# Kernel optimization log

Hardware: AMD Instinct MI355X
Metric: run time of the kernel (lower is better)

Reference implementation:

```python
import jax, jax.numpy as jnp
import numpy as np

B, NPG, HID, HEADS, L = 8, 512, 128, 8, 4
N = B * NPG
E = 16384
EDIM = HID // 4  # edge_dim = hidden_dim // 4 = 32


def _ln(x, g, b):
    m = x.mean(-1, keepdims=True)
    v = ((x - m) ** 2).mean(-1, keepdims=True)
    return (x - m) / jnp.sqrt(v + 1e-5) * g + b


def setup_inputs() -> dict:
    key = jax.random.key(0)
    ks = jax.random.split(key, 24)
    s = 0.05
    epg = E // B
    base = jnp.repeat(jnp.arange(B) * NPG, epg)
    src = base + jax.random.randint(ks[0], (E,), 0, NPG)
    dst = base + jax.random.randint(ks[1], (E,), 0, NPG)
    d = {
        'x': jax.random.randint(ks[2], (N, 1), 0, 100),
        'edge_index': jnp.stack([src, dst]),
        'edge_attr': jax.random.normal(ks[3], (E, 1), jnp.float32),
        'batch': jnp.repeat(jnp.arange(B), NPG),
        'atom_emb': jax.random.normal(ks[4], (100, HID)) * s,
        'edge_w': jax.random.normal(ks[5], (1, EDIM)) * s,
        'edge_b': jnp.zeros((EDIM,)),
        'wq': jax.random.normal(ks[6], (L, HID, HEADS * HID)) * s,
        'bq': jnp.zeros((L, HEADS * HID)),
        'wk': jax.random.normal(ks[7], (L, HID, HEADS * HID)) * s,
        'bk': jnp.zeros((L, HEADS * HID)),
        'wv': jax.random.normal(ks[8], (L, HID, HEADS * HID)) * s,
        'bv': jnp.zeros((L, HEADS * HID)),
        'we': jax.random.normal(ks[9], (L, EDIM, HEADS * HID)) * s,
        'wskip': jax.random.normal(ks[10], (L, HID, HID)) * s,
        'bskip': jnp.zeros((L, HID)),
        'ln_g': jnp.ones((L, HID)),
        'ln_b': jnp.zeros((L, HID)),
        'mha_in_w': jax.random.normal(ks[11], (HID, 3 * HID)) * s,
        'mha_in_b': jnp.zeros((3 * HID,)),
        'mha_out_w': jax.random.normal(ks[12], (HID, HID)) * s,
        'mha_out_b': jnp.zeros((HID,)),
        'w1': jax.random.normal(ks[13], (HID, HID)) * s,
        'b1': jnp.zeros((HID,)),
        'w2': jax.random.normal(ks[14], (HID, HID // 2)) * s,
        'b2': jnp.zeros((HID // 2,)),
        'w3': jax.random.normal(ks[15], (HID // 2, 3)) * s,
        'b3': jnp.zeros((3,)),
    }
    return d


def reference(x, edge_index, edge_attr, batch, atom_emb, edge_w, edge_b,
              wq, bq, wk, bk, wv, bv, we, wskip, bskip, ln_g, ln_b,
              mha_in_w, mha_in_b, mha_out_w, mha_out_b, w1, b1, w2, b2, w3, b3):
    src, dst = edge_index[0], edge_index[1]
    h = atom_emb[x[:, 0]]                       # [N, HID]
    e = edge_attr @ edge_w + edge_b             # [E, EDIM]
    scale = 1.0 / jnp.sqrt(jnp.float32(HID))    # per-head channel dim = HID
    for i in range(L):
        res = h
        q = (h @ wq[i] + bq[i]).reshape(N, HEADS, HID)
        k = (h @ wk[i] + bk[i]).reshape(N, HEADS, HID)
        v = (h @ wv[i] + bv[i]).reshape(N, HEADS, HID)
        ee = (e @ we[i]).reshape(E, HEADS, HID)
        kj = k[src] + ee                        # [E, HEADS, HID]
        vj = v[src] + ee
        logits = jnp.einsum('ehd,ehd->eh', q[dst], kj) * scale
        m = jax.ops.segment_max(logits, dst, num_segments=N)
        a = jnp.exp(logits - m[dst])
        z = jax.ops.segment_sum(a, dst, num_segments=N)
        a = a / (z[dst] + 1e-16)                # edge softmax per target node
        agg = jax.ops.segment_sum(a[:, :, None] * vj, dst, num_segments=N)
        out = agg.mean(axis=1) + h @ wskip[i] + bskip[i]  # concat=False + root skip
        h = jax.nn.gelu(_ln(out + res, ln_g[i], ln_b[i]), approximate=False)
    # equal-size graphs: ragged->padded conversion is a plain reshape, no padding
    p = h.reshape(B, NPG, HID)
    qkv = p @ mha_in_w + mha_in_b               # [B, n, 3*HID]
    hd = HID // HEADS
    q, k, v = [t.reshape(B, NPG, HEADS, hd).transpose(0, 2, 1, 3)
               for t in jnp.split(qkv, 3, axis=-1)]
    att = jax.nn.softmax(jnp.einsum('bhqd,bhkd->bhqk', q, k) / jnp.sqrt(jnp.float32(hd)), axis=-1)
    o = jnp.einsum('bhqk,bhkd->bhqd', att, v).transpose(0, 2, 1, 3).reshape(B, NPG, HID)
    o = (o @ mha_out_w + mha_out_b).reshape(N, HID)
    y = jax.nn.gelu(o @ w1 + b1, approximate=False)
    y = jax.nn.gelu(y @ w2 + b2, approximate=False)
    return y @ w3 + b3                          # [N, 3]
```

## Files before the change

kernel.cpp:

```cpp
#include <hip/hip_runtime.h>
#include <hip/hip_bf16.h>
#include <math.h>

#define NN 4096
#define NE 16384
#define NLAYERS 4

#define WT_STRIDE 442368

typedef __attribute__((ext_vector_type(8))) short bf16x8;
typedef __attribute__((ext_vector_type(4))) float floatx4;

__device__ __forceinline__ float gelu_f(float x) {
  return 0.5f * x * (1.0f + erff(x * 0.70710678118654752440f));
}

__device__ __forceinline__ void bsplit(float a, unsigned short& hi, unsigned short& lo) {
  __hip_bfloat16 h16 = __float2bfloat16(a);
  hi = *(unsigned short*)&h16;
  const float r = a - __bfloat162float(h16);
  __hip_bfloat16 l16 = __float2bfloat16(r);
  lo = *(unsigned short*)&l16;
}

union F16U { float4 v4[4]; float f[16]; };

__global__ void k_init(const int* __restrict__ x, const float* __restrict__ atom_emb,
                       const float* __restrict__ edge_attr, const float* __restrict__ edge_w,
                       const float* __restrict__ edge_b, float* __restrict__ h,
                       float* __restrict__ ef, int* __restrict__ counts,
                       unsigned short* __restrict__ hhi, unsigned short* __restrict__ hlo) {
  const int idx = blockIdx.x * 256 + threadIdx.x;
  const float hv = atom_emb[x[idx >> 7] * 128 + (idx & 127)];
  h[idx] = hv;
  bsplit(hv, hhi[idx], hlo[idx]);
  ef[idx] = edge_attr[idx >> 5] * edge_w[idx & 31] + edge_b[idx & 31];
  if (idx < NN) counts[idx] = 0;
}

__global__ void k_hist(const int* __restrict__ eidx, int* __restrict__ counts) {
  const int e = blockIdx.x * 256 + threadIdx.x;
  if (e < NE) atomicAdd(&counts[eidx[NE + e]], 1);
}

__global__ void k_scan(const int* __restrict__ counts, int* __restrict__ offs,
                       int* __restrict__ heads) {
  __shared__ int tmp[1024];
  const int t = threadIdx.x;
  const int c0 = counts[t*4], c1 = counts[t*4+1], c2 = counts[t*4+2], c3 = counts[t*4+3];
  const int s = c0 + c1 + c2 + c3;
  tmp[t] = s; __syncthreads();
  for (int off = 1; off < 1024; off <<= 1) {
    int v = (t >= off) ? tmp[t - off] : 0;
    __syncthreads();
    tmp[t] += v;
    __syncthreads();
  }
  int base = tmp[t] - s;
  offs[t*4]   = base;                heads[t*4]   = base;
  offs[t*4+1] = base + c0;           heads[t*4+1] = base + c0;
  offs[t*4+2] = base + c0 + c1;      heads[t*4+2] = base + c0 + c1;
  offs[t*4+3] = base + c0 + c1 + c2; heads[t*4+3] = base + c0 + c1 + c2;
  if (t == 1023) offs[NN] = tmp[1023];
}

__global__ void k_scatter(const int* __restrict__ eidx, int* __restrict__ heads,
                          int* __restrict__ elist) {
  const int e = blockIdx.x * 256 + threadIdx.x;
  if (e < NE) {
    int p = atomicAdd(&heads[eidx[NE + e]], 1);
    elist[p] = e;
  }
}

__global__ __launch_bounds__(256) void k_wcvt(
    const float* __restrict__ wq, const float* __restrict__ wk,
    const float* __restrict__ wv, const float* __restrict__ wsk,
    unsigned short* __restrict__ wthi, unsigned short* __restrict__ wtlo) {
  const int z = blockIdx.z;
  const int layer = z >> 2, mat = z & 3;
  int NC; const float* W; int woff;
  if (mat == 0)      { NC = 1024; W = wq  + (size_t)layer * 131072; woff = 0; }
  else if (mat == 1) { NC = 1024; W = wk  + (size_t)layer * 131072; woff = 131072; }
  else if (mat == 2) { NC = 1024; W = wv  + (size_t)layer * 131072; woff = 262144; }
  else               { NC = 128;  W = wsk + (size_t)layer * 16384;  woff = 393216; }
  const int c0 = blockIdx.x * 64;
  if (c0 >= NC) return;
  const int k0 = blockIdx.y * 64;
  __shared__ unsigned short th[64][65], tl[64][65];
  const int t = threadIdx.x;
  for (int i = t; i < 4096; i += 256) {
    const int kk = i >> 6, c = i & 63;
    bsplit(W[(size_t)(k0 + kk) * NC + c0 + c], th[kk][c], tl[kk][c]);
  }
  __syncthreads();
  unsigned short* oh = wthi + (size_t)layer * WT_STRIDE + woff;
  unsigned short* ol = wtlo + (size_t)layer * WT_STRIDE + woff;
  for (int i = t; i < 4096; i += 256) {
    const int n = i >> 6, k = i & 63;
    oh[(size_t)(c0 + n) * 128 + k0 + k] = th[k][n];
    ol[(size_t)(c0 + n) * 128 + k0 + k] = tl[k][n];
  }
}

__global__ __launch_bounds__(256) void k_wqe(
    const float* __restrict__ wq, const float* __restrict__ bq,
    const float* __restrict__ we, unsigned short* __restrict__ wthi,
    unsigned short* __restrict__ wtlo, float* __restrict__ bqe) {
  const int layer = blockIdx.x >> 3, hh = blockIdx.x & 7;
  const float* wq_l = wq + (size_t)layer * 131072;
  const float* we_l = we + (size_t)layer * 32768;
  const float* bq_l = bq + (size_t)layer * 1024;
  __shared__ float wqS[128][132];
  __shared__ float weS[32][132];
  const int t = threadIdx.x;
  for (int i = t; i < 4096; i += 256) {
    const int d = i >> 5, dd4 = (i & 31) << 2;
    *(float4*)&wqS[d][dd4] = *(const float4*)&wq_l[(size_t)d * 1024 + hh * 128 + dd4];
  }
  for (int i = t; i < 1024; i += 256) {
    const int c = i >> 5, dd4 = (i & 31) << 2;
    *(float4*)&weS[c][dd4] = *(const float4*)&we_l[(size_t)c * 1024 + hh * 128 + dd4];
  }
  __syncthreads();
  const int d = t & 127, cg = t >> 7;
  float acc[16];
  #pragma unroll
  for (int cc = 0; cc < 16; cc++) acc[cc] = 0.f;
  for (int dd = 0; dd < 128; dd++) {
    const float a = wqS[d][dd];
    #pragma unroll
    for (int cc = 0; cc < 16; cc++)
      acc[cc] += a * weS[cg * 16 + cc][dd];
  }
  unsigned short* oh = wthi + (size_t)layer * WT_STRIDE + 409600;
  unsigned short* ol = wtlo + (size_t)layer * WT_STRIDE + 409600;
  #pragma unroll
  for (int cc = 0; cc < 16; cc++) {
    const int j = hh * 32 + cg * 16 + cc;
    unsigned short hi, lo;
    bsplit(acc[cc], hi, lo);
    oh[(size_t)j * 128 + d] = hi;
    ol[(size_t)j * 128 + d] = lo;
  }
  if (t < 32) {
    float s = 0.f;
    for (int dd = 0; dd < 128; dd++) s += bq_l[hh * 128 + dd] * weS[t][dd];
    bqe[layer * 256 + hh * 32 + t] = s;
  }
}

__global__ __launch_bounds__(256) void k_mfqkv(
    const unsigned short* __restrict__ hhi, const unsigned short* __restrict__ hlo,
    const unsigned short* __restrict__ wth, const unsigned short* __restrict__ wtl,
    const float* __restrict__ bq, const float* __restrict__ bk,
    const float* __restrict__ bv, const float* __restrict__ bsk,
    const float* __restrict__ bqe_l,
    float* __restrict__ qb, float* __restrict__ kb,
    float* __restrict__ vb, float* __restrict__ skb, float* __restrict__ qeb) {
  const int z = blockIdx.z;
  int NC; const float* bias; float* C; int woff;
  if (z == 0)      { NC = 1024; bias = bq;    C = qb;  woff = 0; }
  else if (z == 1) { NC = 1024; bias = bk;    C = kb;  woff = 131072; }
  else if (z == 2) { NC = 1024; bias = bv;    C = vb;  woff = 262144; }
  else if (z == 3) { NC = 128;  bias = bsk;   C = skb; woff = 393216; }
  else             { NC = 256;  bias = bqe_l; C = qeb; woff = 409600; }
  const int c0 = blockIdx.x * 64;
  if (c0 >= NC) return;
  __shared__ unsigned short Ah[64][136], Al[64][136], Wh[64][136], Wl[64][136];
  const int t = threadIdx.x;
  const int n0 = blockIdx.y * 64;
  for (int i = t; i < 1024; i += 256) {
    const int r = i >> 4, c8 = (i & 15) << 3;
    *(uint4*)&Ah[r][c8] = *(const uint4*)&hhi[(size_t)(n0 + r) * 128 + c8];
    *(uint4*)&Al[r][c8] = *(const uint4*)&hlo[(size_t)(n0 + r) * 128 + c8];
    *(uint4*)&Wh[r][c8] = *(const uint4*)&wth[woff + (size_t)(c0 + r) * 128 + c8];
    *(uint4*)&Wl[r][c8] = *(const uint4*)&wtl[woff + (size_t)(c0 + r) * 128 + c8];
  }
  __syncthreads();
  const int w = t >> 6, l = t & 63;
  const int quad = l >> 4, lm = l & 15;
  floatx4 acc[4] = {{0.f,0.f,0.f,0.f},{0.f,0.f,0.f,0.f},{0.f,0.f,0.f,0.f},{0.f,0.f,0.f,0.f}};
  #pragma unroll
  for (int kc = 0; kc < 4; kc++) {
    const int ko = kc * 32 + quad * 8;
    const bf16x8 ah = *(const bf16x8*)&Ah[w * 16 + lm][ko];
    const bf16x8 al = *(const bf16x8*)&Al[w * 16 + lm][ko];
    #pragma unroll
    for (int ct = 0; ct < 4; ct++) {
      const bf16x8 bh = *(const bf16x8*)&Wh[ct * 16 + lm][ko];
      const bf16x8 bl = *(const bf16x8*)&Wl[ct * 16 + lm][ko];
      acc[ct] = __builtin_amdgcn_mfma_f32_16x16x32_bf16(ah, bh, acc[ct], 0, 0, 0);
      acc[ct] = __builtin_amdgcn_mfma_f32_16x16x32_bf16(ah, bl, acc[ct], 0, 0, 0);
      acc[ct] = __builtin_amdgcn_mfma_f32_16x16x32_bf16(al, bh, acc[ct], 0, 0, 0);
    }
  }
  #pragma unroll
  for (int ct = 0; ct < 4; ct++) {
    const int col = c0 + ct * 16 + lm;
    const float bb = bias[col];
    #pragma unroll
    for (int r = 0; r < 4; r++) {
      const int row = n0 + w * 16 + quad * 4 + r;
      C[(size_t)row * NC + col] = acc[ct][r] + bb;
    }
  }
}

__global__ __launch_bounds__(256) void k_gemm2(const float* __restrict__ A,
                                               const float* __restrict__ W,
                                               const float* __restrict__ bias,
                                               float* __restrict__ C, int NC, int gelu) {
  __shared__ float As[128][65];
  __shared__ float Ws[128][64];
  const int t = threadIdx.x;
  const int n0 = blockIdx.y * 64, c0 = blockIdx.x * 64;
  for (int i = t; i < 2048; i += 256) {
    const int r = i & 63, k4 = (i >> 6) << 2;
    const float4 a = *(const float4*)&A[(size_t)(n0 + r) * 128 + k4];
    As[k4+0][r] = a.x; As[k4+1][r] = a.y; As[k4+2][r] = a.z; As[k4+3][r] = a.w;
  }
  for (int i = t; i < 2048; i += 256) {
    const int kk = i >> 4, c4 = (i & 15) << 2;
    *(float4*)&Ws[kk][c4] = *(const float4*)&W[(size_t)kk * NC + c0 + c4];
  }
  __syncthreads();
  const int tr = (t >> 4) << 2;
  const int tc = (t & 15) << 2;
  float acc[4][4];
  #pragma unroll
  for (int i = 0; i < 4; i++)
    #pragma unroll
    for (int j = 0; j < 4; j++) acc[i][j] = 0.f;
  #pragma unroll 8
  for (int k = 0; k < 128; k++) {
    const float4 av = *(const float4*)&As[k][tr];
    const float4 wv = *(const float4*)&Ws[k][tc];
    acc[0][0] += av.x*wv.x; acc[0][1] += av.x*wv.y; acc[0][2] += av.x*wv.z; acc[0][3] += av.x*wv.w;
    acc[1][0] += av.y*wv.x; acc[1][1] += av.y*wv.y; acc[1][2] += av.y*wv.z; acc[1][3] += av.y*wv.w;
    acc[2][0] += av.z*wv.x; acc[2][1] += av.z*wv.y; acc[2][2] += av.z*wv.z; acc[2][3] += av.z*wv.w;
    acc[3][0] += av.w*wv.x; acc[3][1] += av.w*wv.y; acc[3][2] += av.w*wv.z; acc[3][3] += av.w*wv.w;
  }
  const float4 bb = *(const float4*)&bias[c0 + tc];
  #pragma unroll
  for (int i = 0; i < 4; i++) {
    float4 v;
    v.x = acc[i][0] + bb.x; v.y = acc[i][1] + bb.y;
    v.z = acc[i][2] + bb.z; v.w = acc[i][3] + bb.w;
    if (gelu) { v.x = gelu_f(v.x); v.y = gelu_f(v.y); v.z = gelu_f(v.z); v.w = gelu_f(v.w); }
    *(float4*)&C[(size_t)(n0 + tr + i) * NC + c0 + tc] = v;
  }
}

__global__ __launch_bounds__(256) void k_corr(const float* __restrict__ sbuf,
                                              const float* __restrict__ we_l,
                                              float* __restrict__ corrb) {
  __shared__ float As[32][256];
  __shared__ float Ws[128][64];
  const int t = threadIdx.x;
  const int n0 = blockIdx.y * 32, c0 = blockIdx.x * 64;
  for (int i = t; i < 2048; i += 256) {
    const int r = i >> 6, c4 = (i & 63) << 2;
    *(float4*)&As[r][c4] = *(const float4*)&sbuf[(size_t)(n0 + r) * 256 + c4];
  }
  const int tx = t & 63, ty = t >> 6;
  float acc[8] = {0.f,0.f,0.f,0.f,0.f,0.f,0.f,0.f};
  for (int kc = 0; kc < 2; kc++) {
    __syncthreads();
    for (int i = t; i < 2048; i += 256) {
      const int kk = i >> 4, c4 = (i & 15) << 2;
      const int k = kc * 128 + kk;
      const int hh = k >> 5, c = k & 31;
      *(float4*)&Ws[kk][c4] = *(const float4*)&we_l[(size_t)c * 1024 + hh * 128 + c0 + c4];
    }
    __syncthreads();
    for (int kk = 0; kk < 128; kk += 4) {
      const float w0 = Ws[kk+0][tx];
      const float w1 = Ws[kk+1][tx];
      const float w2 = Ws[kk+2][tx];
      const float w3 = Ws[kk+3][tx];
      #pragma unroll
      for (int j = 0; j < 8; j++) {
        const float4 a = *(const float4*)&As[ty*8 + j][kc*128 + kk];
        acc[j] += a.x*w0 + a.y*w1 + a.z*w2 + a.w*w3;
      }
    }
  }
  #pragma unroll
  for (int j = 0; j < 8; j++)
    corrb[(size_t)(n0 + ty*8 + j) * 128 + c0 + tx] = acc[j];
}

__global__ __launch_bounds__(64) void k_edge(const float* __restrict__ qb,
                                             const float* __restrict__ kb,
                                             const float* __restrict__ vb,
                                             const float* __restrict__ qe,
                                             const float* __restrict__ ef,
                                             const int* __restrict__ offs,
                                             const int* __restrict__ elist,
                                             const int* __restrict__ eidx,
                                             float* __restrict__ accm,
                                             float* __restrict__ sbuf) {
  const int n = blockIdx.x;
  const int lane = threadIdx.x;
  const int hh = lane >> 3, s8 = lane & 7;
  const int d0 = hh * 128 + s8 * 16;
  F16U qv;
  {
    const float4* qp = (const float4*)(qb + (size_t)n * 1024 + d0);
    #pragma unroll
    for (int i = 0; i < 4; i++) qv.v4[i] = qp[i];
  }
  const float4 qe4 = *(const float4*)(qe + (size_t)n * 256 + hh * 32 + s8 * 4);
  float m = -INFINITY, z = 0.f;
  float acc[16];
  #pragma unroll
  for (int i = 0; i < 16; i++) acc[i] = 0.f;
  float sx = 0.f, sy = 0.f, sz = 0.f, sw = 0.f;
  const int e0 = offs[n], e1 = offs[n + 1];
  for (int tt = e0; tt < e1; tt++) {
    const int e = elist[tt];
    const int src = eidx[e];
    F16U kv;
    {
      const float4* kp = (const float4*)(kb + (size_t)src * 1024 + d0);
      #pragma unroll
      for (int i = 0; i < 4; i++) kv.v4[i] = kp[i];
    }
    const float4 ef4 = *(const float4*)(ef + (size_t)e * 32 + s8 * 4);
    float p0 = qe4.x*ef4.x + qe4.y*ef4.y;
    float p1 = qe4.z*ef4.z + qe4.w*ef4.w;
    float p2 = 0.f, p3 = 0.f;
    #pragma unroll
    for (int i = 0; i < 4; i++) {
      p0 += qv.f[i]      * kv.f[i];
      p1 += qv.f[4 + i]  * kv.f[4 + i];
      p2 += qv.f[8 + i]  * kv.f[8 + i];
      p3 += qv.f[12 + i] * kv.f[12 + i];
    }
    float p = (p0 + p1) + (p2 + p3);
    p += __shfl_xor(p, 1);
    p += __shfl_xor(p, 2);
    p += __shfl_xor(p, 4);
    const float logit = p * 0.08838834764831845f;
    if (logit > m + 8.f) {
      const float f = __expf(m - logit);
      z *= f; sx *= f; sy *= f; sz *= f; sw *= f;
      #pragma unroll
      for (int i = 0; i < 16; i++) acc[i] *= f;
      m = logit;
    }
    const float w = __expf(logit - m);
    z += w;
    F16U vv;
    {
      const float4* vp = (const float4*)(vb + (size_t)src * 1024 + d0);
      #pragma unroll
      for (int i = 0; i < 4; i++) vv.v4[i] = vp[i];
    }
    #pragma unroll
    for (int i = 0; i < 16; i++) acc[i] += w * vv.f[i];
    sx += w * ef4.x; sy += w * ef4.y;
    sz += w * ef4.z; sw += w * ef4.w;
  }
  const float inv = 1.f / (z + 1e-16f);
  *(float4*)(sbuf + (size_t)n * 256 + hh * 32 + s8 * 4) =
      make_float4(sx * inv, sy * inv, sz * inv, sw * inv);
  F16U ov;
  #pragma unroll
  for (int i = 0; i < 16; i++) ov.f[i] = acc[i] * inv;
  #pragma unroll
  for (int mask = 8; mask <= 32; mask <<= 1)
    #pragma unroll
    for (int i = 0; i < 16; i++) ov.f[i] += __shfl_xor(ov.f[i], mask);
  if (hh == 0) {
    #pragma unroll
    for (int i = 0; i < 16; i++) ov.f[i] *= 0.125f;
    float4* ap = (float4*)(accm + (size_t)n * 128 + s8 * 16);
    #pragma unroll
    for (int i = 0; i < 4; i++) ap[i] = ov.v4[i];
  }
}

__global__ __launch_bounds__(128) void k_post2(float* __restrict__ h,
                                               const float* __restrict__ accm,
                                               const float* __restrict__ corrb,
                                               const float* __restrict__ skb,
                                               const float* __restrict__ lng,
                                               const float* __restrict__ lnb,
                                               unsigned short* __restrict__ hhi,
                                               unsigned short* __restrict__ hlo) {
  const int n = blockIdx.x, d = threadIdx.x;
  __shared__ float red[128], stat[2];
  const size_t o = (size_t)n * 128 + d;
  const float out = accm[o] + 0.125f * corrb[o] + skb[o] + h[o];
  red[d] = out; __syncthreads();
  for (int s2 = 64; s2 > 0; s2 >>= 1) { if (d < s2) red[d] += red[d + s2]; __syncthreads(); }
  if (d == 0) stat[0] = red[0] * (1.f / 128.f);
  __syncthreads();
  const float mean = stat[0];
  const float dev = out - mean;
  red[d] = dev * dev; __syncthreads();
  for (int s2 = 64; s2 > 0; s2 >>= 1) { if (d < s2) red[d] += red[d + s2]; __syncthreads(); }
  if (d == 0) stat[1] = red[0] * (1.f / 128.f);
  __syncthreads();
  const float var = stat[1];
  const float y = dev / sqrtf(var + 1e-5f) * lng[d] + lnb[d];
  const float g = gelu_f(y);
  h[o] = g;
  bsplit(g, hhi[o], hlo[o]);
}

__global__ __launch_bounds__(256) void k_attn2b(const float* __restrict__ qkvm,
                                                float* __restrict__ pm,
                                                float* __restrict__ pz,
                                                float* __restrict__ pacc) {
  __shared__ float ks2[64][16];
  __shared__ float vs2[64][16];
  const int ksp = blockIdx.x, qt = blockIdx.y, bh = blockIdx.z;
  const int b = bh >> 3, hh = bh & 7;
  const int t = threadIdx.x;
  const size_t rbase = (size_t)(b * 512 + ksp * 64);
  {
    const int j = t >> 2, d4 = (t & 3) << 2;
    const size_t ro = (rbase + j) * 384 + hh * 16 + d4;
    *(float4*)&ks2[j][d4] = *(const float4*)&qkvm[ro + 128];
    *(float4*)&vs2[j][d4] = *(const float4*)&qkvm[ro + 256];
  }
  __syncthreads();
  const int qrow = qt * 256 + t;
  const int nq = b * 512 + qrow;
  F16U qv;
  {
    const float4* qp = (const float4*)(qkvm + (size_t)nq * 384 + hh * 16);
    #pragma unroll
    for (int i = 0; i < 4; i++) qv.v4[i] = qp[i];
  }
  float m = -INFINITY, z = 0.f;
  float acc[16];
  #pragma unroll
  for (int i = 0; i < 16; i++) acc[i] = 0.f;
  for (int j = 0; j < 64; j += 2) {
    F16U k0, k1, v0, v1;
    {
      const float4* p0 = (const float4*)ks2[j];
      const float4* p1 = (const float4*)ks2[j + 1];
      const float4* q0 = (const float4*)vs2[j];
      const float4* q1 = (const float4*)vs2[j + 1];
      #pragma unroll
      for (int i = 0; i < 4; i++) {
        k0.v4[i] = p0[i]; k1.v4[i] = p1[i];
        v0.v4[i] = q0[i]; v1.v4[i] = q1[i];
      }
    }
    float a0 = 0.f, a1 = 0.f, a2 = 0.f, a3 = 0.f;
    float b0 = 0.f, b1 = 0.f, b2 = 0.f, b3 = 0.f;
    #pragma unroll
    for (int i = 0; i < 4; i++) {
      a0 += qv.f[i]      * k0.f[i];
      a1 += qv.f[4 + i]  * k0.f[4 + i];
      a2 += qv.f[8 + i]  * k0.f[8 + i];
      a3 += qv.f[12 + i] * k0.f[12 + i];
      b0 += qv.f[i]      * k1.f[i];
      b1 += qv.f[4 + i]  * k1.f[4 + i];
      b2 += qv.f[8 + i]  * k1.f[8 + i];
      b3 += qv.f[12 + i] * k1.f[12 + i];
    }
    const float sa = ((a0 + a1) + (a2 + a3)) * 0.25f;
    const float sb = ((b0 + b1) + (b2 + b3)) * 0.25f;
    const float smax = fmaxf(sa, sb);
    if (smax > m + 8.f) {
      const float f = __expf(m - smax);
      z *= f;
      #pragma unroll
      for (int i = 0; i < 16; i++) acc[i] *= f;
      m = smax;
    }
    const float wa = __expf(sa - m);
    const float wb = __expf(sb - m);
    z += wa + wb;
    #pragma unroll
    for (int i = 0; i < 16; i++)
      acc[i] += wa * v0.f[i] + wb * v1.f[i];
  }
  const int p = (bh * 512 + qrow) * 8 + ksp;
  pm[p] = m; pz[p] = z;
  float4* pp = (float4*)&pacc[(size_t)p * 16];
  F16U ov;
  #pragma unroll
  for (int i = 0; i < 16; i++) ov.f[i] = acc[i];
  #pragma unroll
  for (int i = 0; i < 4; i++) pp[i] = ov.v4[i];
}

__global__ void k_amerge(const float* __restrict__ pm, const float* __restrict__ pz,
                         const float* __restrict__ pacc, float* __restrict__ ob) {
  const int idx = blockIdx.x * 256 + threadIdx.x;
  if (idx >= 32768) return;
  const int bh = idx >> 9, qrow = idx & 511;
  const int b = bh >> 3, hh = bh & 7;
  float ms = pm[idx*8];
  #pragma unroll
  for (int s = 1; s < 8; s++) ms = fmaxf(ms, pm[idx*8+s]);
  float wgt[8];
  float z = 0.f;
  #pragma unroll
  for (int s = 0; s < 8; s++) {
    wgt[s] = __expf(pm[idx*8+s] - ms);
    z += pz[idx*8+s] * wgt[s];
  }
  const float inv = 1.f / z;
  float* op = &ob[(size_t)(b * 512 + qrow) * 128 + hh * 16];
  #pragma unroll
  for (int d = 0; d < 16; d++) {
    float o = 0.f;
    #pragma unroll
    for (int s = 0; s < 8; s++)
      o += pacc[(size_t)(idx*8+s) * 16 + d] * wgt[s];
    op[d] = o * inv;
  }
}

__global__ void k_final(const float* __restrict__ y2, const float* __restrict__ w3,
                        const float* __restrict__ b3, float* __restrict__ out) {
  const int idx = blockIdx.x * 256 + threadIdx.x;
  if (idx >= NN * 3) return;
  const int n = idx / 3, j = idx % 3;
  float s = b3[j];
  const float* yp = y2 + (size_t)n * 64;
  #pragma unroll
  for (int c = 0; c < 64; c++) s += yp[c] * w3[c * 3 + j];
  out[idx] = s;
}

extern "C" void kernel_launch(void* const* d_in, const int* in_sizes, int n_in,
                              void* d_out, int out_size, void* d_ws, size_t ws_size,
                              hipStream_t stream) {
  const int*   x         = (const int*)d_in[0];
  const int*   eidx      = (const int*)d_in[1];
  const float* edge_attr = (const float*)d_in[2];
  const float* atom_emb  = (const float*)d_in[4];
  const float* edge_w    = (const float*)d_in[5];
  const float* edge_b    = (const float*)d_in[6];
  const float* wq        = (const float*)d_in[7];
  const float* bq        = (const float*)d_in[8];
  const float* wk        = (const float*)d_in[9];
  const float* bk        = (const float*)d_in[10];
  const float* wv        = (const float*)d_in[11];
  const float* bv        = (const float*)d_in[12];
  const float* we        = (const float*)d_in[13];
  const float* wskip     = (const float*)d_in[14];
  const float* bskip     = (const float*)d_in[15];
  const float* ln_g      = (const float*)d_in[16];
  const float* ln_b      = (const float*)d_in[17];
  const float* mha_in_w  = (const float*)d_in[18];
  const float* mha_in_b  = (const float*)d_in[19];
  const float* mha_out_w = (const float*)d_in[20];
  const float* mha_out_b = (const float*)d_in[21];
  const float* w1        = (const float*)d_in[22];
  const float* b1        = (const float*)d_in[23];
  const float* w2        = (const float*)d_in[24];
  const float* b2        = (const float*)d_in[25];
  const float* w3        = (const float*)d_in[26];
  const float* b3        = (const float*)d_in[27];

  float* ws   = (float*)d_ws;
  float* h    = ws;
  float* ef   = h + 524288;
  float* qb   = ef + 524288;
  float* kb   = qb + 4194304;
  float* vb   = kb + 4194304;
  float* qe   = vb + 4194304;
  float* big  = qe + 1048576;
  float* accm = big;
  float* corrb= big + 524288;
  float* skb  = big + 1048576;
  unsigned short* hhi  = (unsigned short*)(big + 1572864);
  unsigned short* hlo  = hhi + 524288;
  unsigned short* wthi = hlo + 524288;
  unsigned short* wtlo = wthi + 1769472;
  float* sbuf = big + 4194304;
  float* qkvm = qb;
  float* pm   = sbuf;
  float* pz   = sbuf + 262144;
  float* pacc = big;
  float* ob   = kb;
  float* mo   = kb + 524288;
  float* y1   = kb + 1048576;
  float* y2   = kb + 1572864;
  int* counts = (int*)(sbuf + 1048576);
  int* offs   = counts + 4100;
  int* heads  = offs + 4100;
  int* elist  = heads + 4100;
  float* bqe  = (float*)(elist + 16384);

  k_init<<<2048, 256, 0, stream>>>(x, atom_emb, edge_attr, edge_w, edge_b, h, ef, counts,
                                   hhi, hlo);
  k_hist<<<64, 256, 0, stream>>>(eidx, counts);
  k_scan<<<1, 1024, 0, stream>>>(counts, offs, heads);
  k_scatter<<<64, 256, 0, stream>>>(eidx, heads, elist);
  k_wcvt<<<dim3(16, 2, 16), 256, 0, stream>>>(wq, wk, wv, wskip, wthi, wtlo);
  k_wqe<<<32, 256, 0, stream>>>(wq, bq, we, wthi, wtlo, bqe);

  for (int i = 0; i < NLAYERS; i++) {
    const float* bq_i  = bq + (size_t)i * 1024;
    const float* bk_i  = bk + (size_t)i * 1024;
    const float* bv_i  = bv + (size_t)i * 1024;
    const float* we_i  = we + (size_t)i * 32768;
    const float* bsk_i = bskip + (size_t)i * 128;
    const float* g_i   = ln_g + (size_t)i * 128;
    const float* b_i   = ln_b + (size_t)i * 128;
    const unsigned short* wth_i = wthi + (size_t)i * WT_STRIDE;
    const unsigned short* wtl_i = wtlo + (size_t)i * WT_STRIDE;

    k_mfqkv<<<dim3(16, 64, 5), 256, 0, stream>>>(hhi, hlo, wth_i, wtl_i,
                                                 bq_i, bk_i, bv_i, bsk_i, bqe + i * 256,
                                                 qb, kb, vb, skb, qe);
    k_edge<<<4096, 64, 0, stream>>>(qb, kb, vb, qe, ef, offs, elist, eidx, accm, sbuf);
    k_corr<<<dim3(2, 128), 256, 0, stream>>>(sbuf, we_i, corrb);
    k_post2<<<4096, 128, 0, stream>>>(h, accm, corrb, skb, g_i, b_i, hhi, hlo);
  }

  k_gemm2<<<dim3(6, 64), 256, 0, stream>>>(h, mha_in_w, mha_in_b, qkvm, 384, 0);
  k_attn2b<<<dim3(8, 2, 64), 256, 0, stream>>>(qkvm, pm, pz, pacc);
  k_amerge<<<128, 256, 0, stream>>>(pm, pz, pacc, ob);
  k_gemm2<<<dim3(2, 64), 256, 0, stream>>>(ob, mha_out_w, mha_out_b, mo, 128, 0);
  k_gemm2<<<dim3(2, 64), 256, 0, stream>>>(mo, w1, b1, y1, 128, 1);
  k_gemm2<<<dim3(1, 64), 256, 0, stream>>>(y1, w2, b2, y2, 64, 1);
  k_final<<<48, 256, 0, stream>>>(y2, w3, b3, (float*)d_out);
}
```

Measured before the change: 553.3 us.

## Fuse edge-correction GEMM with LayerNorm/GELU post, compact QKV grid, batch edge warps

Merges the per-layer correction GEMM and the residual+LayerNorm+GELU post-processing into one kernel, so the corrb buffer is no longer written and re-read and one launch per layer goes away. The QKV projection grid is flattened to cover only the 54 valid column tiles instead of launching 80 with early exits. The edge kernel now packs four nodes per 256-thread block with a strided node mapping. The fused post kernel runs on only 128 blocks and redoes the correction GEMM for both column halves inside each block, so there is less parallelism for that stage.

Measured after the change: 561.0 us. Within noise of the previous version (+1.4%).

```diff
diff --git a/kernel.cpp b/kernel.cpp
--- a/kernel.cpp
+++ b/kernel.cpp
@@ -158,15 +158,13 @@
     const float* __restrict__ bqe_l,
     float* __restrict__ qb, float* __restrict__ kb,
     float* __restrict__ vb, float* __restrict__ skb, float* __restrict__ qeb) {
-  const int z = blockIdx.z;
-  int NC; const float* bias; float* C; int woff;
-  if (z == 0)      { NC = 1024; bias = bq;    C = qb;  woff = 0; }
-  else if (z == 1) { NC = 1024; bias = bk;    C = kb;  woff = 131072; }
-  else if (z == 2) { NC = 1024; bias = bv;    C = vb;  woff = 262144; }
-  else if (z == 3) { NC = 128;  bias = bsk;   C = skb; woff = 393216; }
-  else             { NC = 256;  bias = bqe_l; C = qeb; woff = 409600; }
-  const int c0 = blockIdx.x * 64;
-  if (c0 >= NC) return;
+  const int xb = blockIdx.x;
+  int NC; const float* bias; float* C; int woff; int c0;
+  if (xb < 16)      { NC = 1024; bias = bq;    C = qb;  woff = 0;      c0 = xb * 64; }
+  else if (xb < 32) { NC = 1024; bias = bk;    C = kb;  woff = 131072; c0 = (xb-16) * 64; }
+  else if (xb < 48) { NC = 1024; bias = bv;    C = vb;  woff = 262144; c0 = (xb-32) * 64; }
+  else if (xb < 50) { NC = 128;  bias = bsk;   C = skb; woff = 393216; c0 = (xb-48) * 64; }
+  else              { NC = 256;  bias = bqe_l; C = qeb; woff = 409600; c0 = (xb-50) * 64; }
   __shared__ unsigned short Ah[64][136], Al[64][136], Wh[64][136], Wl[64][136];
   const int t = threadIdx.x;
   const int n0 = blockIdx.y * 64;
@@ -252,57 +250,99 @@
   }
 }
 
-__global__ __launch_bounds__(256) void k_corr(const float* __restrict__ sbuf,
-                                              const float* __restrict__ we_l,
-                                              float* __restrict__ corrb) {
+__global__ __launch_bounds__(256) void k_corrpost(
+    const float* __restrict__ sbuf, const float* __restrict__ we_l,
+    const float* __restrict__ accm, const float* __restrict__ skb,
+    const float* __restrict__ lng, const float* __restrict__ lnb,
+    float* __restrict__ h,
+    unsigned short* __restrict__ hhi, unsigned short* __restrict__ hlo) {
   __shared__ float As[32][256];
   __shared__ float Ws[128][64];
+  __shared__ float sC[32][129];
   const int t = threadIdx.x;
-  const int n0 = blockIdx.y * 32, c0 = blockIdx.x * 64;
+  const int n0 = blockIdx.x * 32;
   for (int i = t; i < 2048; i += 256) {
     const int r = i >> 6, c4 = (i & 63) << 2;
     *(float4*)&As[r][c4] = *(const float4*)&sbuf[(size_t)(n0 + r) * 256 + c4];
   }
   const int tx = t & 63, ty = t >> 6;
-  float acc[8] = {0.f,0.f,0.f,0.f,0.f,0.f,0.f,0.f};
-  for (int kc = 0; kc < 2; kc++) {
-    __syncthreads();
-    for (int i = t; i < 2048; i += 256) {
-      const int kk = i >> 4, c4 = (i & 15) << 2;
-      const int k = kc * 128 + kk;
-      const int hh = k >> 5, c = k & 31;
-      *(float4*)&Ws[kk][c4] = *(const float4*)&we_l[(size_t)c * 1024 + hh * 128 + c0 + c4];
-    }
-    __syncthreads();
-    for (int kk = 0; kk < 128; kk += 4) {
-      const float w0 = Ws[kk+0][tx];
-      const float w1 = Ws[kk+1][tx];
-      const float w2 = Ws[kk+2][tx];
-      const float w3 = Ws[kk+3][tx];
-      #pragma unroll
-      for (int j = 0; j < 8; j++) {
-        const float4 a = *(const float4*)&As[ty*8 + j][kc*128 + kk];
-        acc[j] += a.x*w0 + a.y*w1 + a.z*w2 + a.w*w3;
+  float acc[2][8];
+  #pragma unroll
+  for (int cc = 0; cc < 2; cc++)
+    #pragma unroll
+    for (int j = 0; j < 8; j++) acc[cc][j] = 0.f;
+  #pragma unroll
+  for (int cc = 0; cc < 2; cc++) {
+    const int c0 = cc * 64;
+    for (int kc = 0; kc < 2; kc++) {
+      __syncthreads();
+      for (int i = t; i < 2048; i += 256) {
+        const int kk = i >> 4, c4 = (i & 15) << 2;
+        const int k = kc * 128 + kk;
+        const int hh = k >> 5, c = k & 31;
+        *(float4*)&Ws[kk][c4] = *(const float4*)&we_l[(size_t)c * 1024 + hh * 128 + c0 + c4];
       }
-    }
-  }
-  #pragma unroll
-  for (int j = 0; j < 8; j++)
-    corrb[(size_t)(n0 + ty*8 + j) * 128 + c0 + tx] = acc[j];
-}
-
-__global__ __launch_bounds__(64) void k_edge(const float* __restrict__ qb,
-                                             const float* __restrict__ kb,
-                                             const float* __restrict__ vb,
-                                             const float* __restrict__ qe,
-                                             const float* __restrict__ ef,
-                                             const int* __restrict__ offs,
-                                             const int* __restrict__ elist,
-                                             const int* __restrict__ eidx,
-                                             float* __restrict__ accm,
-                                             float* __restrict__ sbuf) {
-  const int n = blockIdx.x;
-  const int lane = threadIdx.x;
+      __syncthreads();
+      for (int kk = 0; kk < 128; kk += 4) {
+        const float w0 = Ws[kk+0][tx];
+        const float w1 = Ws[kk+1][tx];
+        const float w2 = Ws[kk+2][tx];
+        const float w3 = Ws[kk+3][tx];
+        #pragma unroll
+        for (int j = 0; j < 8; j++) {
+          const float4 a = *(const float4*)&As[ty*8 + j][kc*128 + kk];
+          acc[cc][j] += a.x*w0 + a.y*w1 + a.z*w2 + a.w*w3;
+        }
+      }
+    }
+  }
+  #pragma unroll
+  for (int j = 0; j < 8; j++) {
+    sC[ty*8 + j][tx]      = acc[0][j];
+    sC[ty*8 + j][64 + tx] = acc[1][j];
+  }
+  __syncthreads();
+  const int w = t >> 6, lane = t & 63;
+  const float g0c = lng[lane], g1c = lng[64 + lane];
+  const float b0c = lnb[lane], b1c = lnb[64 + lane];
+  for (int j = 0; j < 8; j++) {
+    const int nn = w * 8 + j;
+    const size_t o = (size_t)(n0 + nn) * 128;
+    const float v0 = accm[o + lane]      + 0.125f * sC[nn][lane]      + skb[o + lane]      + h[o + lane];
+    const float v1 = accm[o + 64 + lane] + 0.125f * sC[nn][64 + lane] + skb[o + 64 + lane] + h[o + 64 + lane];
+    float s = v0 + v1;
+    #pragma unroll
+    for (int mask = 1; mask <= 32; mask <<= 1) s += __shfl_xor(s, mask);
+    const float mean = s * (1.f / 128.f);
+    const float d0 = v0 - mean, d1 = v1 - mean;
+    float vs = d0*d0 + d1*d1;
+    #pragma unroll
+    for (int mask = 1; mask <= 32; mask <<= 1) vs += __shfl_xor(vs, mask);
+    const float rstd = 1.f / sqrtf(vs * (1.f / 128.f) + 1e-5f);
+    const float y0 = d0 * rstd * g0c + b0c;
+    const float y1 = d1 * rstd * g1c + b1c;
+    const float r0 = gelu_f(y0);
+    const float r1 = gelu_f(y1);
+    h[o + lane] = r0;
+    h[o + 64 + lane] = r1;
+    bsplit(r0, hhi[o + lane], hlo[o + lane]);
+    bsplit(r1, hhi[o + 64 + lane], hlo[o + 64 + lane]);
+  }
+}
+
+__global__ __launch_bounds__(256) void k_edge(const float* __restrict__ qb,
+                                              const float* __restrict__ kb,
+                                              const float* __restrict__ vb,
+                                              const float* __restrict__ qe,
+                                              const float* __restrict__ ef,
+                                              const int* __restrict__ offs,
+                                              const int* __restrict__ elist,
+                                              const int* __restrict__ eidx,
+                                              float* __restrict__ accm,
+                                              float* __restrict__ sbuf) {
+  const int wid = threadIdx.x >> 6;
+  const int n = (blockIdx.x & 7) * 512 + (blockIdx.x >> 3) * 4 + wid;
+  const int lane = threadIdx.x & 63;
   const int hh = lane >> 3, s8 = lane & 7;
   const int d0 = hh * 128 + s8 * 16;
   F16U qv;
@@ -380,35 +420,6 @@
     #pragma unroll
     for (int i = 0; i < 4; i++) ap[i] = ov.v4[i];
   }
-}
-
-__global__ __launch_bounds__(128) void k_post2(float* __restrict__ h,
-                                               const float* __restrict__ accm,
-                                               const float* __restrict__ corrb,
-                                               const float* __restrict__ skb,
-                                               const float* __restrict__ lng,
-                                               const float* __restrict__ lnb,
-                                               unsigned short* __restrict__ hhi,
-                                               unsigned short* __restrict__ hlo) {
-  const int n = blockIdx.x, d = threadIdx.x;
-  __shared__ float red[128], stat[2];
-  const size_t o = (size_t)n * 128 + d;
-  const float out = accm[o] + 0.125f * corrb[o] + skb[o] + h[o];
-  red[d] = out; __syncthreads();
-  for (int s2 = 64; s2 > 0; s2 >>= 1) { if (d < s2) red[d] += red[d + s2]; __syncthreads(); }
-  if (d == 0) stat[0] = red[0] * (1.f / 128.f);
-  __syncthreads();
-  const float mean = stat[0];
-  const float dev = out - mean;
-  red[d] = dev * dev; __syncthreads();
-  for (int s2 = 64; s2 > 0; s2 >>= 1) { if (d < s2) red[d] += red[d + s2]; __syncthreads(); }
-  if (d == 0) stat[1] = red[0] * (1.f / 128.f);
-  __syncthreads();
-  const float var = stat[1];
-  const float y = dev / sqrtf(var + 1e-5f) * lng[d] + lnb[d];
-  const float g = gelu_f(y);
-  h[o] = g;
-  bsplit(g, hhi[o], hlo[o]);
 }
 
 __global__ __launch_bounds__(256) void k_attn2b(const float* __restrict__ qkvm,
@@ -573,7 +584,6 @@
   float* qe   = vb + 4194304;
   float* big  = qe + 1048576;
   float* accm = big;
-  float* corrb= big + 524288;
   float* skb  = big + 1048576;
   unsigned short* hhi  = (unsigned short*)(big + 1572864);
   unsigned short* hlo  = hhi + 524288;
@@ -613,12 +623,11 @@
     const unsigned short* wth_i = wthi + (size_t)i * WT_STRIDE;
     const unsigned short* wtl_i = wtlo + (size_t)i * WT_STRIDE;
 
-    k_mfqkv<<<dim3(16, 64, 5), 256, 0, stream>>>(hhi, hlo, wth_i, wtl_i,
-                                                 bq_i, bk_i, bv_i, bsk_i, bqe + i * 256,
-                                                 qb, kb, vb, skb, qe);
-    k_edge<<<4096, 64, 0, stream>>>(qb, kb, vb, qe, ef, offs, elist, eidx, accm, sbuf);
-    k_corr<<<dim3(2, 128), 256, 0, stream>>>(sbuf, we_i, corrb);
-    k_post2<<<4096, 128, 0, stream>>>(h, accm, corrb, skb, g_i, b_i, hhi, hlo);
+    k_mfqkv<<<dim3(54, 64), 256, 0, stream>>>(hhi, hlo, wth_i, wtl_i,
+                                              bq_i, bk_i, bv_i, bsk_i, bqe + i * 256,
+                                              qb, kb, vb, skb, qe);
+    k_edge<<<1024, 256, 0, stream>>>(qb, kb, vb, qe, ef, offs, elist, eidx, accm, sbuf);
+    k_corrpost<<<128, 256, 0, stream>>>(sbuf, we_i, accm, skb, g_i, b_i, h, hhi, hlo);
   }
 
   k_gemm2<<<dim3(6, 64), 256, 0, stream>>>(h, mha_in_w, mha_in_b, qkvm, 384, 0);
```
